# Optimization experiments

Measured on AMD Instinct MI355X. Metric: run time of the kernel, lower is better.

Reference implementation:

```python
import jax, jax.numpy as jnp
import numpy as np

N, T0, T1 = 2, 4, 8
H, W = 128, 128
PD, AD = 4, 4
Z_POS, Z_APP = PD * PD, AD * AD
Z = Z_POS + Z_APP
KS, STRIDE, ROUTINGS = 3, 1, 3


def psquash(p, axis):
    return p / jnp.max(jnp.abs(p), axis=axis, keepdims=True)


def matwo_squash(p, axis):
    sq = jnp.sum(p * p, axis=axis, keepdims=True)
    return sq / (1.0 + sq) * p / jnp.sqrt(sq + 1e-9)


def setup_inputs() -> dict:
    key = jax.random.key(0)
    ks = jax.random.split(key, 5)
    return {
        "x": jax.random.normal(ks[0], (N, T0, Z, H, W), jnp.float32),
        "W_conv": jax.random.normal(ks[1], (T0, KS, KS, 1, T1), jnp.float32) * 0.1,
        "W_pos": jax.random.normal(ks[2], (T0, Z_POS, T1), jnp.float32) * 0.1,
        "W_app": jax.random.normal(ks[3], (T0, Z_APP, T1), jnp.float32) * 0.1,
        "b_app": jax.random.normal(ks[4], (T0, T1), jnp.float32) * 0.1,
    }


def _forward(x, W_conv, W_pos, W_app, b_app):
    n, t0, z0, h, w = x.shape
    t1 = W_conv.shape[-1]
    # per-input-capsule 2D conv: channels folded into batch, 1 -> t1 channels
    xt = x.transpose(1, 0, 2, 3, 4).reshape(t0, n * z0, h, w, 1)
    conv = jax.vmap(lambda u, k: jax.lax.conv_general_dilated(
        u, k, (STRIDE, STRIDE), 'SAME',
        dimension_numbers=('NHWC', 'HWIO', 'NHWC')))(xt, W_conv)
    h1, w1 = conv.shape[2], conv.shape[3]
    # [t0, N, z0, H1, W1, t1] -> [t0, N, H1, W1, t1, z0] -> flatten (t1,z0)
    u = conv.reshape(t0, n, z0, h1, w1, t1).transpose(0, 1, 3, 4, 5, 2)
    flat = u.reshape(t0, n, h1, w1, t1 * z0)
    # faithful replication of the original tf.split on the flattened (t1*z0) axis
    u_pos = flat[..., :t1 * Z_POS].reshape(t0, n, h1, w1, t1, PD, PD)
    u_app = flat[..., t1 * Z_POS:].reshape(t0, n, h1, w1, t1, AD, AD)

    # pose transform matrices: l2-normalize columns (axis=-2), coordinate addition
    mult_pos = W_pos.reshape(t0, t1, PD, PD)
    mult_pos = mult_pos / jnp.sqrt(
        jnp.maximum(jnp.sum(mult_pos * mult_pos, axis=-2, keepdims=True), 1e-12))
    coord = jnp.zeros((h1, w1, 1, PD, PD), x.dtype)
    coord = coord.at[:, :, 0, -1, 0].add(jnp.arange(w1, dtype=x.dtype)[None, :] / w1)
    coord = coord.at[:, :, 0, -1, 1].add(jnp.arange(h1, dtype=x.dtype)[:, None] / h1)
    mult_pos_hw = mult_pos[:, None, None] + coord[None]  # [t0,h1,w1,t1,PD,PD]
    u_hat_pos = jnp.einsum('cnhwtij,chwtjk->cnhwtik', u_pos, mult_pos_hw)

    mult_app = W_app.reshape(t0, t1, AD, AD)
    u_app = u_app + b_app[:, None, None, None, :, None, None]
    u_hat_app = jnp.einsum('cnhwtij,ctjk->cnhwtik', u_app, mult_app)

    u_hat = jnp.concatenate(
        [u_hat_pos.reshape(t0, n, h1, w1, t1, Z_POS),
         u_hat_app.reshape(t0, n, h1, w1, t1, Z_APP)], axis=-1)
    u_hat = u_hat.transpose(1, 5, 2, 3, 0, 4)  # [N, z1, H1, W1, t0, t1]

    # dual routing (sigmoid coupling, separate pos/app agreement)
    uh_pos, uh_app = u_hat[:, :Z_POS], u_hat[:, Z_POS:]
    b = jnp.zeros((n, h1, w1, t0, t1), x.dtype)
    for _ in range(ROUTINGS - 1):
        r = jax.nn.sigmoid(b)
        p = jnp.einsum('nzhwct,nhwct->nzhwt', u_hat, r)
        v_pos = psquash(p[:, :Z_POS], axis=1)
        v_app = matwo_squash(p[:, Z_POS:], axis=1)
        rout = (jnp.einsum('nzhwct,nzhwt->nhwct', uh_pos, v_pos)
                * jnp.einsum('nzhwct,nzhwt->nhwct', uh_app, v_app))
        b = b + rout
    c = jax.nn.sigmoid(b)
    p = jnp.einsum('nzhwct,nhwct->nzhwt', u_hat, c)
    v = jnp.concatenate([psquash(p[:, :Z_POS], axis=1),
                         matwo_squash(p[:, Z_POS:], axis=1)], axis=1)
    return v.transpose(0, 4, 1, 2, 3)  # [N, t1, z1, H1, W1]


def reference(x, W_conv, W_pos, W_app, b_app):
    return _forward(x, W_conv, W_pos, W_app, b_app)
```

## Files before the change

kernel.cpp:

```cpp
#include <hip/hip_runtime.h>
#include <cmath>


#define TH 2
#define TW 8
#define XR (TH + 2)
#define XC (TW + 2)
#define ZPAD 36

__device__ __forceinline__ float qsum4(float v) {
    int a = __builtin_amdgcn_mov_dpp(__float_as_int(v), 0xB1, 0xF, 0xF, true);
    v += __int_as_float(a);
    int b = __builtin_amdgcn_mov_dpp(__float_as_int(v), 0x4E, 0xF, 0xF, true);
    v += __int_as_float(b);
    return v;
}

__global__ __launch_bounds__(256, 3)
void caps_fused(const float* __restrict__ x,
                const float* __restrict__ Wc,
                const float* __restrict__ Wp,
                const float* __restrict__ Wa,
                const float* __restrict__ ba,
                float* __restrict__ out)
{
    __shared__ float xs[XR][XC][4][ZPAD];

    const int tid = threadIdx.x;
    const int n  = blockIdx.z;
    const int h0 = blockIdx.y * TH;
    const int w0 = blockIdx.x * TW;

    for (int e = tid; e < 128 * XR * XC; e += 256) {
        int col = e % XC;
        int tmp = e / XC;
        int row = tmp % XR;
        int cz  = tmp / XR;
        int gh = h0 - 1 + row;
        int gw = w0 - 1 + col;
        float v = 0.0f;
        if ((unsigned)gh < 128u && (unsigned)gw < 128u)
            v = x[(((size_t)(n * 128 + cz)) << 14) + (gh << 7) + gw];
        int z = cz & 31;
        int s = (row * XC + col) & 7;
        xs[row][col][cz >> 5][((((z >> 2) & 7) ^ s) << 2) | (z & 3)] = v;
    }

    const int p    = tid >> 5;
    const int lane = tid & 31;
    const int c    = lane & 3;
    const int t    = lane >> 2;
    const int chp  = t >> 1;
    const int q0   = (t & 1) << 2;

    float wp9[9], wa9[9];
#pragma unroll
    for (int i = 0; i < 9; ++i) {
        wp9[i] = Wc[(c * 9 + i) * 8 + chp];
        wa9[i] = Wc[(c * 9 + i) * 8 + 4 + chp];
    }
    float Mp[16], Ma[16];
#pragma unroll
    for (int q = 0; q < 16; ++q) {
        Mp[q] = Wp[c * 128 + t * 16 + q];
        Ma[q] = Wa[c * 128 + t * 16 + q];
    }
#pragma unroll
    for (int k = 0; k < 4; ++k) {
        float s = Mp[k] * Mp[k] + Mp[4 + k] * Mp[4 + k]
                + Mp[8 + k] * Mp[8 + k] + Mp[12 + k] * Mp[12 + k];
        float inv = __builtin_amdgcn_rsqf(fmaxf(s, 1e-12f));
        Mp[k] *= inv; Mp[4 + k] *= inv; Mp[8 + k] *= inv; Mp[12 + k] *= inv;
    }
    const float bap = ba[c * 8 + t];
    const float wx  = (float)(w0 + p) * (1.0f / 128.0f);

    __syncthreads();

    for (int g = 0; g < TH; ++g) {
        float up[16], ua[16];
#pragma unroll
        for (int q = 0; q < 16; ++q) { up[q] = 0.0f; ua[q] = 0.0f; }
#pragma unroll
        for (int dy = 0; dy < 3; ++dy) {
#pragma unroll
            for (int dx = 0; dx < 3; ++dx) {
                const int rr = g + dy, cc = p + dx;
                const int s = (rr * XC + cc) & 7;
                const float* bp = &xs[rr][cc][c][0];
                float xv[16];
                *(float4*)&xv[0]  = *(const float4*)(bp + (((q0 | 0) ^ s) << 2));
                *(float4*)&xv[4]  = *(const float4*)(bp + (((q0 | 1) ^ s) << 2));
                *(float4*)&xv[8]  = *(const float4*)(bp + (((q0 | 2) ^ s) << 2));
                *(float4*)&xv[12] = *(const float4*)(bp + (((q0 | 3) ^ s) << 2));
                const float w1 = wp9[dy * 3 + dx];
                const float w2 = wa9[dy * 3 + dx];
#pragma unroll
                for (int q = 0; q < 16; ++q) {
                    up[q] += xv[q] * w1;
                    ua[q] += xv[q] * w2;
                }
            }
        }

        const float hy = (float)(h0 + g) * (1.0f / 128.0f);
        float uh[32];
#pragma unroll
        for (int i = 0; i < 4; ++i) {
#pragma unroll
            for (int k = 0; k < 4; ++k) {
                uh[i * 4 + k] = up[i * 4 + 0] * Mp[k]
                              + up[i * 4 + 1] * Mp[4 + k]
                              + up[i * 4 + 2] * Mp[8 + k]
                              + up[i * 4 + 3] * Mp[12 + k];
            }
            uh[i * 4 + 0] += up[i * 4 + 3] * wx;
            uh[i * 4 + 1] += up[i * 4 + 3] * hy;
        }
#pragma unroll
        for (int i = 0; i < 4; ++i) {
            const float a0 = ua[i * 4 + 0] + bap;
            const float a1 = ua[i * 4 + 1] + bap;
            const float a2 = ua[i * 4 + 2] + bap;
            const float a3 = ua[i * 4 + 3] + bap;
#pragma unroll
            for (int k = 0; k < 4; ++k)
                uh[16 + i * 4 + k] = a0 * Ma[k] + a1 * Ma[4 + k]
                                   + a2 * Ma[8 + k] + a3 * Ma[12 + k];
        }

        float bacc = 0.0f;
#pragma unroll
        for (int it = 0; it < 3; ++it) {
            const float r = __builtin_amdgcn_rcpf(1.0f + __expf(-bacc));
            float pz[32];
#pragma unroll
            for (int zz = 0; zz < 32; ++zz)
                pz[zz] = qsum4(uh[zz] * r);

            float mx = 0.0f;
#pragma unroll
            for (int zz = 0; zz < 16; ++zz) mx = fmaxf(mx, fabsf(pz[zz]));
            const float invm = __builtin_amdgcn_rcpf(mx);
            float sq = 0.0f;
#pragma unroll
            for (int zz = 16; zz < 32; ++zz) sq += pz[zz] * pz[zz];
            const float fac = sq * __builtin_amdgcn_rcpf(1.0f + sq)
                                 * __builtin_amdgcn_rsqf(sq + 1e-9f);

            if (it < 2) {
                float dp = 0.0f, da = 0.0f;
#pragma unroll
                for (int zz = 0; zz < 16; ++zz) dp += uh[zz] * pz[zz];
#pragma unroll
                for (int zz = 16; zz < 32; ++zz) da += uh[zz] * pz[zz];
                bacc += (dp * invm) * (da * fac);
            } else if (c == 0) {
                const int row = h0 + g;
                float* ob = out + (((size_t)((n * 8 + t) * 32)) << 14)
                                + (row << 7) + (w0 + p);
#pragma unroll
                for (int zz = 0; zz < 16; ++zz)
                    ob[((size_t)zz) << 14] = pz[zz] * invm;
#pragma unroll
                for (int zz = 16; zz < 32; ++zz)
                    ob[((size_t)zz) << 14] = pz[zz] * fac;
            }
        }
    }
}

extern "C" void kernel_launch(void* const* d_in, const int* in_sizes, int n_in,
                              void* d_out, int out_size, void* d_ws, size_t ws_size,
                              hipStream_t stream) {
    const float* x  = (const float*)d_in[0];
    const float* Wc = (const float*)d_in[1];
    const float* Wp = (const float*)d_in[2];
    const float* Wa = (const float*)d_in[3];
    const float* ba = (const float*)d_in[4];
    float* out = (float*)d_out;

    dim3 grid(128 / TW, 128 / TH, 2);
    caps_fused<<<grid, 256, 0, stream>>>(x, Wc, Wp, Wa, ba, out);
}
```

Measured before the change: 128.6 us.

## Split pose and appearance halves across wave halves with larger row tile

Each 64-lane wave now handles one output position, with the lower 32 lanes computing the pose half and the upper 32 the appearance half. Before, a 32-lane group computed both halves. This halves the per-thread register arrays and the conv FMAs per thread. The routing agreement product is combined across halves with a cross-lane shuffle. The block grows to 512 threads and the tile height to 4 rows, which reuses more of each shared-memory halo load but enlarges the LDS footprint per block.

After: 137.7 us. 1.07x slower.

```diff
diff --git a/kernel.cpp b/kernel.cpp
--- a/kernel.cpp
+++ b/kernel.cpp
@@ -2,11 +2,10 @@
 #include <cmath>
 
 
-#define TH 2
+#define TH 4
 #define TW 8
 #define XR (TH + 2)
 #define XC (TW + 2)
-#define ZPAD 36
 
 __device__ __forceinline__ float qsum4(float v) {
     int a = __builtin_amdgcn_mov_dpp(__float_as_int(v), 0xB1, 0xF, 0xF, true);
@@ -16,7 +15,7 @@
     return v;
 }
 
-__global__ __launch_bounds__(256, 3)
+__global__ __launch_bounds__(512, 4)
 void caps_fused(const float* __restrict__ x,
                 const float* __restrict__ Wc,
                 const float* __restrict__ Wp,
@@ -24,14 +23,14 @@
                 const float* __restrict__ ba,
                 float* __restrict__ out)
 {
-    __shared__ float xs[XR][XC][4][ZPAD];
+    __shared__ float xs[XR][XC][4][36];
 
     const int tid = threadIdx.x;
     const int n  = blockIdx.z;
     const int h0 = blockIdx.y * TH;
     const int w0 = blockIdx.x * TW;
 
-    for (int e = tid; e < 128 * XR * XC; e += 256) {
+    for (int e = tid; e < 128 * XR * XC; e += 512) {
         int col = e % XC;
         int tmp = e / XC;
         int row = tmp % XR;
@@ -43,44 +42,45 @@
             v = x[(((size_t)(n * 128 + cz)) << 14) + (gh << 7) + gw];
         int z = cz & 31;
         int s = (row * XC + col) & 7;
-        xs[row][col][cz >> 5][((((z >> 2) & 7) ^ s) << 2) | (z & 3)] = v;
+        xs[row][col][cz >> 5][(((z >> 2) ^ s) << 2) | (z & 3)] = v;
     }
 
-    const int p    = tid >> 5;
-    const int lane = tid & 31;
+    const int p    = tid >> 6;
+    const int lane = tid & 63;
     const int c    = lane & 3;
-    const int t    = lane >> 2;
-    const int chp  = t >> 1;
+    const int t    = (lane >> 2) & 7;
+    const int half = lane >> 5;
+    const int ch   = (half << 2) + (t >> 1);
     const int q0   = (t & 1) << 2;
 
-    float wp9[9], wa9[9];
+    float w9[9];
 #pragma unroll
-    for (int i = 0; i < 9; ++i) {
-        wp9[i] = Wc[(c * 9 + i) * 8 + chp];
-        wa9[i] = Wc[(c * 9 + i) * 8 + 4 + chp];
+    for (int i = 0; i < 9; ++i)
+        w9[i] = Wc[(c * 9 + i) * 8 + ch];
+
+    const float* Wsel = half ? Wa : Wp;
+    float M[16];
+#pragma unroll
+    for (int q = 0; q < 16; ++q)
+        M[q] = Wsel[c * 128 + t * 16 + q];
+    if (half == 0) {
+#pragma unroll
+        for (int k = 0; k < 4; ++k) {
+            float s = M[k] * M[k] + M[4 + k] * M[4 + k]
+                    + M[8 + k] * M[8 + k] + M[12 + k] * M[12 + k];
+            float inv = __builtin_amdgcn_rsqf(fmaxf(s, 1e-12f));
+            M[k] *= inv; M[4 + k] *= inv; M[8 + k] *= inv; M[12 + k] *= inv;
+        }
     }
-    float Mp[16], Ma[16];
-#pragma unroll
-    for (int q = 0; q < 16; ++q) {
-        Mp[q] = Wp[c * 128 + t * 16 + q];
-        Ma[q] = Wa[c * 128 + t * 16 + q];
-    }
-#pragma unroll
-    for (int k = 0; k < 4; ++k) {
-        float s = Mp[k] * Mp[k] + Mp[4 + k] * Mp[4 + k]
-                + Mp[8 + k] * Mp[8 + k] + Mp[12 + k] * Mp[12 + k];
-        float inv = __builtin_amdgcn_rsqf(fmaxf(s, 1e-12f));
-        Mp[k] *= inv; Mp[4 + k] *= inv; Mp[8 + k] *= inv; Mp[12 + k] *= inv;
-    }
-    const float bap = ba[c * 8 + t];
-    const float wx  = (float)(w0 + p) * (1.0f / 128.0f);
+    const float badd = half ? ba[c * 8 + t] : 0.0f;
+    const float wxe  = half ? 0.0f : (float)(w0 + p) * (1.0f / 128.0f);
 
     __syncthreads();
 
     for (int g = 0; g < TH; ++g) {
-        float up[16], ua[16];
+        float up[16];
 #pragma unroll
-        for (int q = 0; q < 16; ++q) { up[q] = 0.0f; ua[q] = 0.0f; }
+        for (int q = 0; q < 16; ++q) up[q] = 0.0f;
 #pragma unroll
         for (int dy = 0; dy < 3; ++dy) {
 #pragma unroll
@@ -88,83 +88,76 @@
                 const int rr = g + dy, cc = p + dx;
                 const int s = (rr * XC + cc) & 7;
                 const float* bp = &xs[rr][cc][c][0];
-                float xv[16];
-                *(float4*)&xv[0]  = *(const float4*)(bp + (((q0 | 0) ^ s) << 2));
-                *(float4*)&xv[4]  = *(const float4*)(bp + (((q0 | 1) ^ s) << 2));
-                *(float4*)&xv[8]  = *(const float4*)(bp + (((q0 | 2) ^ s) << 2));
-                *(float4*)&xv[12] = *(const float4*)(bp + (((q0 | 3) ^ s) << 2));
-                const float w1 = wp9[dy * 3 + dx];
-                const float w2 = wa9[dy * 3 + dx];
+                const float w = w9[dy * 3 + dx];
 #pragma unroll
-                for (int q = 0; q < 16; ++q) {
-                    up[q] += xv[q] * w1;
-                    ua[q] += xv[q] * w2;
+                for (int i = 0; i < 4; ++i) {
+                    float4 v4 = *(const float4*)(bp + (((q0 | i) ^ s) << 2));
+                    up[i * 4 + 0] += v4.x * w;
+                    up[i * 4 + 1] += v4.y * w;
+                    up[i * 4 + 2] += v4.z * w;
+                    up[i * 4 + 3] += v4.w * w;
                 }
             }
         }
 
-        const float hy = (float)(h0 + g) * (1.0f / 128.0f);
-        float uh[32];
+        const float hye = half ? 0.0f : (float)(h0 + g) * (1.0f / 128.0f);
+        float uh[16];
 #pragma unroll
         for (int i = 0; i < 4; ++i) {
-#pragma unroll
-            for (int k = 0; k < 4; ++k) {
-                uh[i * 4 + k] = up[i * 4 + 0] * Mp[k]
-                              + up[i * 4 + 1] * Mp[4 + k]
-                              + up[i * 4 + 2] * Mp[8 + k]
-                              + up[i * 4 + 3] * Mp[12 + k];
-            }
-            uh[i * 4 + 0] += up[i * 4 + 3] * wx;
-            uh[i * 4 + 1] += up[i * 4 + 3] * hy;
-        }
-#pragma unroll
-        for (int i = 0; i < 4; ++i) {
-            const float a0 = ua[i * 4 + 0] + bap;
-            const float a1 = ua[i * 4 + 1] + bap;
-            const float a2 = ua[i * 4 + 2] + bap;
-            const float a3 = ua[i * 4 + 3] + bap;
+            const float a0 = up[i * 4 + 0] + badd;
+            const float a1 = up[i * 4 + 1] + badd;
+            const float a2 = up[i * 4 + 2] + badd;
+            const float a3 = up[i * 4 + 3] + badd;
 #pragma unroll
             for (int k = 0; k < 4; ++k)
-                uh[16 + i * 4 + k] = a0 * Ma[k] + a1 * Ma[4 + k]
-                                   + a2 * Ma[8 + k] + a3 * Ma[12 + k];
+                uh[i * 4 + k] = a0 * M[k] + a1 * M[4 + k]
+                              + a2 * M[8 + k] + a3 * M[12 + k];
+            uh[i * 4 + 0] += a3 * wxe;
+            uh[i * 4 + 1] += a3 * hye;
         }
 
         float bacc = 0.0f;
 #pragma unroll
         for (int it = 0; it < 3; ++it) {
             const float r = __builtin_amdgcn_rcpf(1.0f + __expf(-bacc));
-            float pz[32];
+            float pz[16];
 #pragma unroll
-            for (int zz = 0; zz < 32; ++zz)
+            for (int zz = 0; zz < 16; ++zz)
                 pz[zz] = qsum4(uh[zz] * r);
 
-            float mx = 0.0f;
-#pragma unroll
-            for (int zz = 0; zz < 16; ++zz) mx = fmaxf(mx, fabsf(pz[zz]));
-            const float invm = __builtin_amdgcn_rcpf(mx);
+            float m01 = fmaxf(fabsf(pz[0]), fabsf(pz[1]));
+            float m23 = fmaxf(fabsf(pz[2]), fabsf(pz[3]));
+            float m45 = fmaxf(fabsf(pz[4]), fabsf(pz[5]));
+            float m67 = fmaxf(fabsf(pz[6]), fabsf(pz[7]));
+            float m89 = fmaxf(fabsf(pz[8]), fabsf(pz[9]));
+            float mab = fmaxf(fabsf(pz[10]), fabsf(pz[11]));
+            float mcd = fmaxf(fabsf(pz[12]), fabsf(pz[13]));
+            float mef = fmaxf(fabsf(pz[14]), fabsf(pz[15]));
+            float mx = fmaxf(fmaxf(fmaxf(m01, m23), fmaxf(m45, m67)),
+                             fmaxf(fmaxf(m89, mab), fmaxf(mcd, mef)));
             float sq = 0.0f;
 #pragma unroll
-            for (int zz = 16; zz < 32; ++zz) sq += pz[zz] * pz[zz];
-            const float fac = sq * __builtin_amdgcn_rcpf(1.0f + sq)
-                                 * __builtin_amdgcn_rsqf(sq + 1e-9f);
+            for (int zz = 0; zz < 16; ++zz) sq += pz[zz] * pz[zz];
+
+            const float invm = __builtin_amdgcn_rcpf(mx);
+            const float fac  = sq * __builtin_amdgcn_rcpf(1.0f + sq)
+                                  * __builtin_amdgcn_rsqf(sq + 1e-9f);
+            const float scale = half ? fac : invm;
 
             if (it < 2) {
-                float dp = 0.0f, da = 0.0f;
+                float dp = 0.0f;
 #pragma unroll
                 for (int zz = 0; zz < 16; ++zz) dp += uh[zz] * pz[zz];
-#pragma unroll
-                for (int zz = 16; zz < 32; ++zz) da += uh[zz] * pz[zz];
-                bacc += (dp * invm) * (da * fac);
+                const float s1 = dp * scale;
+                const float s2 = __shfl_xor(s1, 32, 64);
+                bacc += s1 * s2;
             } else if (c == 0) {
                 const int row = h0 + g;
-                float* ob = out + (((size_t)((n * 8 + t) * 32)) << 14)
+                float* ob = out + (((size_t)((n * 8 + t) * 32 + half * 16)) << 14)
                                 + (row << 7) + (w0 + p);
 #pragma unroll
                 for (int zz = 0; zz < 16; ++zz)
-                    ob[((size_t)zz) << 14] = pz[zz] * invm;
-#pragma unroll
-                for (int zz = 16; zz < 32; ++zz)
-                    ob[((size_t)zz) << 14] = pz[zz] * fac;
+                    ob[((size_t)zz) << 14] = pz[zz] * scale;
             }
         }
     }
@@ -181,5 +174,5 @@
     float* out = (float*)d_out;
 
     dim3 grid(128 / TW, 128 / TH, 2);
-    caps_fused<<<grid, 256, 0, stream>>>(x, Wc, Wp, Wa, ba, out);
+    caps_fused<<<grid, 512, 0, stream>>>(x, Wc, Wp, Wa, ba, out);
 }
```

## Split each capsule's pose rows across two half-waves and stage weights in LDS

Applied to the files above, without the earlier changes.

Each output pixel now uses a full 64-lane wavefront instead of 32 lanes. The two halves each compute half of the pose rows, and partial max, square-sum and dot products are combined with a cross-half shuffle. Transform matrices and conv weights move from per-thread registers into shared memory, with a swizzled layout to avoid bank conflicts. The tile shape changes to 4x4 and the occupancy hint is dropped. Together these cut per-thread register use and duplicated work, in exchange for extra shuffles and LDS reads.

After: 142.7 us. 1.11x slower.

```diff
diff --git a/kernel.cpp b/kernel.cpp
--- a/kernel.cpp
+++ b/kernel.cpp
@@ -2,11 +2,10 @@
 #include <cmath>
 
 
-#define TH 2
-#define TW 8
+#define TH 4
+#define TW 4
 #define XR (TH + 2)
 #define XC (TW + 2)
-#define ZPAD 36
 
 __device__ __forceinline__ float qsum4(float v) {
     int a = __builtin_amdgcn_mov_dpp(__float_as_int(v), 0xB1, 0xF, 0xF, true);
@@ -16,7 +15,7 @@
     return v;
 }
 
-__global__ __launch_bounds__(256, 3)
+__global__ __launch_bounds__(256)
 void caps_fused(const float* __restrict__ x,
                 const float* __restrict__ Wc,
                 const float* __restrict__ Wp,
@@ -24,7 +23,9 @@
                 const float* __restrict__ ba,
                 float* __restrict__ out)
 {
-    __shared__ float xs[XR][XC][4][ZPAD];
+    __shared__ float xs[XR][XC][4][36];
+    __shared__ float Mt[32][32];
+    __shared__ float Wl[288];
 
     const int tid = threadIdx.x;
     const int n  = blockIdx.z;
@@ -43,128 +44,136 @@
             v = x[(((size_t)(n * 128 + cz)) << 14) + (gh << 7) + gw];
         int z = cz & 31;
         int s = (row * XC + col) & 7;
-        xs[row][col][cz >> 5][((((z >> 2) & 7) ^ s) << 2) | (z & 3)] = v;
+        xs[row][col][cz >> 5][(((z >> 2) ^ s) << 2) | (z & 3)] = v;
+    }
+    for (int e = tid; e < 288; e += 256) {
+        int sel = e & 1;
+        int chp = (e >> 1) & 3;
+        int ctap = e >> 3;
+        Wl[e] = Wc[ctap * 8 + (sel ? 4 + chp : chp)];
+    }
+    if (tid < 32) {
+        const int ctx = tid;
+        const int cc = ctx & 3, tt = ctx >> 2;
+        float Mp[16], Ma[16];
+#pragma unroll
+        for (int q = 0; q < 16; ++q) {
+            Mp[q] = Wp[cc * 128 + tt * 16 + q];
+            Ma[q] = Wa[cc * 128 + tt * 16 + q];
+        }
+#pragma unroll
+        for (int k = 0; k < 4; ++k) {
+            float s2 = Mp[k] * Mp[k] + Mp[4 + k] * Mp[4 + k]
+                     + Mp[8 + k] * Mp[8 + k] + Mp[12 + k] * Mp[12 + k];
+            float inv = __builtin_amdgcn_rsqf(fmaxf(s2, 1e-12f));
+            Mp[k] *= inv; Mp[4 + k] *= inv; Mp[8 + k] *= inv; Mp[12 + k] *= inv;
+        }
+        const int swz = ctx & 7;
+#pragma unroll
+        for (int j = 0; j < 4; ++j)
+#pragma unroll
+            for (int k = 0; k < 4; ++k) {
+                Mt[ctx][((j ^ swz) << 2) + k]       = Mp[j * 4 + k];
+                Mt[ctx][(((4 + j) ^ swz) << 2) + k] = Ma[j * 4 + k];
+            }
     }
 
-    const int p    = tid >> 5;
-    const int lane = tid & 31;
+    const int p    = tid >> 6;
+    const int lane = tid & 63;
     const int c    = lane & 3;
-    const int t    = lane >> 2;
+    const int t    = (lane >> 2) & 7;
+    const int qp   = lane >> 5;
+    const int ct   = lane & 31;
+    const int sw   = ct & 7;
     const int chp  = t >> 1;
-    const int q0   = (t & 1) << 2;
+    const int zsel = (t & 1) << 2;
 
-    float wp9[9], wa9[9];
-#pragma unroll
-    for (int i = 0; i < 9; ++i) {
-        wp9[i] = Wc[(c * 9 + i) * 8 + chp];
-        wa9[i] = Wc[(c * 9 + i) * 8 + 4 + chp];
-    }
-    float Mp[16], Ma[16];
-#pragma unroll
-    for (int q = 0; q < 16; ++q) {
-        Mp[q] = Wp[c * 128 + t * 16 + q];
-        Ma[q] = Wa[c * 128 + t * 16 + q];
-    }
-#pragma unroll
-    for (int k = 0; k < 4; ++k) {
-        float s = Mp[k] * Mp[k] + Mp[4 + k] * Mp[4 + k]
-                + Mp[8 + k] * Mp[8 + k] + Mp[12 + k] * Mp[12 + k];
-        float inv = __builtin_amdgcn_rsqf(fmaxf(s, 1e-12f));
-        Mp[k] *= inv; Mp[4 + k] *= inv; Mp[8 + k] *= inv; Mp[12 + k] *= inv;
-    }
     const float bap = ba[c * 8 + t];
     const float wx  = (float)(w0 + p) * (1.0f / 128.0f);
 
     __syncthreads();
 
     for (int g = 0; g < TH; ++g) {
-        float up[16], ua[16];
-#pragma unroll
-        for (int q = 0; q < 16; ++q) { up[q] = 0.0f; ua[q] = 0.0f; }
+        float u0[4] = {0,0,0,0}, u1[4] = {0,0,0,0};
+        float a0[4] = {0,0,0,0}, a1[4] = {0,0,0,0};
+        const int gq0 = zsel | qp;
+        const int gq1 = zsel | (qp + 2);
 #pragma unroll
         for (int dy = 0; dy < 3; ++dy) {
 #pragma unroll
             for (int dx = 0; dx < 3; ++dx) {
-                const int rr = g + dy, cc = p + dx;
-                const int s = (rr * XC + cc) & 7;
-                const float* bp = &xs[rr][cc][c][0];
-                float xv[16];
-                *(float4*)&xv[0]  = *(const float4*)(bp + (((q0 | 0) ^ s) << 2));
-                *(float4*)&xv[4]  = *(const float4*)(bp + (((q0 | 1) ^ s) << 2));
-                *(float4*)&xv[8]  = *(const float4*)(bp + (((q0 | 2) ^ s) << 2));
-                *(float4*)&xv[12] = *(const float4*)(bp + (((q0 | 3) ^ s) << 2));
-                const float w1 = wp9[dy * 3 + dx];
-                const float w2 = wa9[dy * 3 + dx];
-#pragma unroll
-                for (int q = 0; q < 16; ++q) {
-                    up[q] += xv[q] * w1;
-                    ua[q] += xv[q] * w2;
-                }
+                const int rr = g + dy, cc2 = p + dx;
+                const int s  = (rr * XC + cc2) & 7;
+                const float2 wv = *(const float2*)&Wl[((c * 9 + dy * 3 + dx) * 4 + chp) * 2];
+                const float* bpx = &xs[rr][cc2][c][0];
+                const float4 x0 = *(const float4*)(bpx + ((gq0 ^ s) << 2));
+                const float4 x1 = *(const float4*)(bpx + ((gq1 ^ s) << 2));
+                u0[0] += x0.x * wv.x; u0[1] += x0.y * wv.x; u0[2] += x0.z * wv.x; u0[3] += x0.w * wv.x;
+                a0[0] += x0.x * wv.y; a0[1] += x0.y * wv.y; a0[2] += x0.z * wv.y; a0[3] += x0.w * wv.y;
+                u1[0] += x1.x * wv.x; u1[1] += x1.y * wv.x; u1[2] += x1.z * wv.x; u1[3] += x1.w * wv.x;
+                a1[0] += x1.x * wv.y; a1[1] += x1.y * wv.y; a1[2] += x1.z * wv.y; a1[3] += x1.w * wv.y;
             }
         }
 
+#pragma unroll
+        for (int j = 0; j < 4; ++j) { a0[j] += bap; a1[j] += bap; }
         const float hy = (float)(h0 + g) * (1.0f / 128.0f);
-        float uh[32];
+        float uh[16];
 #pragma unroll
-        for (int i = 0; i < 4; ++i) {
+        for (int q = 0; q < 16; ++q) uh[q] = 0.0f;
 #pragma unroll
-            for (int k = 0; k < 4; ++k) {
-                uh[i * 4 + k] = up[i * 4 + 0] * Mp[k]
-                              + up[i * 4 + 1] * Mp[4 + k]
-                              + up[i * 4 + 2] * Mp[8 + k]
-                              + up[i * 4 + 3] * Mp[12 + k];
-            }
-            uh[i * 4 + 0] += up[i * 4 + 3] * wx;
-            uh[i * 4 + 1] += up[i * 4 + 3] * hy;
+        for (int j = 0; j < 4; ++j) {
+            const float4 mp = *(const float4*)&Mt[ct][(j ^ sw) << 2];
+            const float4 ma = *(const float4*)&Mt[ct][((4 + j) ^ sw) << 2];
+            uh[0]  += u0[j] * mp.x; uh[1]  += u0[j] * mp.y; uh[2]  += u0[j] * mp.z; uh[3]  += u0[j] * mp.w;
+            uh[4]  += u1[j] * mp.x; uh[5]  += u1[j] * mp.y; uh[6]  += u1[j] * mp.z; uh[7]  += u1[j] * mp.w;
+            uh[8]  += a0[j] * ma.x; uh[9]  += a0[j] * ma.y; uh[10] += a0[j] * ma.z; uh[11] += a0[j] * ma.w;
+            uh[12] += a1[j] * ma.x; uh[13] += a1[j] * ma.y; uh[14] += a1[j] * ma.z; uh[15] += a1[j] * ma.w;
         }
-#pragma unroll
-        for (int i = 0; i < 4; ++i) {
-            const float a0 = ua[i * 4 + 0] + bap;
-            const float a1 = ua[i * 4 + 1] + bap;
-            const float a2 = ua[i * 4 + 2] + bap;
-            const float a3 = ua[i * 4 + 3] + bap;
-#pragma unroll
-            for (int k = 0; k < 4; ++k)
-                uh[16 + i * 4 + k] = a0 * Ma[k] + a1 * Ma[4 + k]
-                                   + a2 * Ma[8 + k] + a3 * Ma[12 + k];
-        }
+        uh[0] += u0[3] * wx;  uh[1] += u0[3] * hy;
+        uh[4] += u1[3] * wx;  uh[5] += u1[3] * hy;
 
         float bacc = 0.0f;
 #pragma unroll
         for (int it = 0; it < 3; ++it) {
             const float r = __builtin_amdgcn_rcpf(1.0f + __expf(-bacc));
-            float pz[32];
+            float pp[8], pa[8];
+            float mxl = 0.0f, sql = 0.0f, dpl = 0.0f, dal = 0.0f;
 #pragma unroll
-            for (int zz = 0; zz < 32; ++zz)
-                pz[zz] = qsum4(uh[zz] * r);
-
-            float mx = 0.0f;
+            for (int m = 0; m < 8; ++m) {
+                const float pv = qsum4(uh[m] * r);
+                pp[m] = pv;
+                mxl = fmaxf(mxl, fabsf(pv));
+                dpl += uh[m] * pv;
+            }
 #pragma unroll
-            for (int zz = 0; zz < 16; ++zz) mx = fmaxf(mx, fabsf(pz[zz]));
+            for (int m = 0; m < 8; ++m) {
+                const float pv = qsum4(uh[8 + m] * r);
+                pa[m] = pv;
+                sql += pv * pv;
+                dal += uh[8 + m] * pv;
+            }
+            const float mx = fmaxf(mxl, __shfl_xor(mxl, 32, 64));
+            const float sq = sql + __shfl_xor(sql, 32, 64);
             const float invm = __builtin_amdgcn_rcpf(mx);
-            float sq = 0.0f;
-#pragma unroll
-            for (int zz = 16; zz < 32; ++zz) sq += pz[zz] * pz[zz];
-            const float fac = sq * __builtin_amdgcn_rcpf(1.0f + sq)
-                                 * __builtin_amdgcn_rsqf(sq + 1e-9f);
-
+            const float fac  = sq * __builtin_amdgcn_rcpf(1.0f + sq)
+                                  * __builtin_amdgcn_rsqf(sq + 1e-9f);
             if (it < 2) {
-                float dp = 0.0f, da = 0.0f;
-#pragma unroll
-                for (int zz = 0; zz < 16; ++zz) dp += uh[zz] * pz[zz];
-#pragma unroll
-                for (int zz = 16; zz < 32; ++zz) da += uh[zz] * pz[zz];
+                const float dp = dpl + __shfl_xor(dpl, 32, 64);
+                const float da = dal + __shfl_xor(dal, 32, 64);
                 bacc += (dp * invm) * (da * fac);
             } else if (c == 0) {
                 const int row = h0 + g;
                 float* ob = out + (((size_t)((n * 8 + t) * 32)) << 14)
                                 + (row << 7) + (w0 + p);
 #pragma unroll
-                for (int zz = 0; zz < 16; ++zz)
-                    ob[((size_t)zz) << 14] = pz[zz] * invm;
+                for (int ii = 0; ii < 2; ++ii)
 #pragma unroll
-                for (int zz = 16; zz < 32; ++zz)
-                    ob[((size_t)zz) << 14] = pz[zz] * fac;
+                    for (int k = 0; k < 4; ++k) {
+                        const int z = (qp + 2 * ii) * 4 + k;
+                        ob[((size_t)z) << 14]        = pp[ii * 4 + k] * invm;
+                        ob[((size_t)(16 + z)) << 14] = pa[ii * 4 + k] * fac;
+                    }
             }
         }
     }
```
